# Kernel optimization log

Measured on AMD Instinct MI355X. Metric: run time of the kernel, lower is better.

## Reference

```python
import jax, jax.numpy as jnp
import numpy as np

D_MODEL = 768
D_FF = 2048
N_EXP = 8
TOP_K = 2


def setup_inputs() -> dict:
    key = jax.random.key(0)
    ks = jax.random.split(key, 8)
    s = 0.02
    inputs = jax.random.normal(ks[0], (4, 2048, D_MODEL), dtype=jnp.float32)
    gate_w = jax.random.normal(ks[1], (D_MODEL, N_EXP), dtype=jnp.float32) * s
    w1 = jax.random.normal(ks[2], (N_EXP, D_MODEL, D_FF), dtype=jnp.float32) * s
    w3 = jax.random.normal(ks[3], (N_EXP, D_MODEL, D_FF), dtype=jnp.float32) * s
    w2 = jax.random.normal(ks[4], (N_EXP, D_FF, D_MODEL), dtype=jnp.float32) * s
    sw1 = jax.random.normal(ks[5], (D_MODEL, D_FF), dtype=jnp.float32) * s
    sw3 = jax.random.normal(ks[6], (D_MODEL, D_FF), dtype=jnp.float32) * s
    sw2 = jax.random.normal(ks[7], (D_FF, D_MODEL), dtype=jnp.float32) * s
    return {"inputs": inputs, "gate_w": gate_w, "w1": w1, "w3": w3, "w2": w2,
            "sw1": sw1, "sw3": sw3, "sw2": sw2}


def _swiglu(x, wa, wb, wc):
    # silu(x @ wa) * (x @ wb) @ wc
    return (jax.nn.silu(x @ wa) * (x @ wb)) @ wc


def reference(inputs, gate_w, w1, w3, w2, sw1, sw3, sw2):
    B, T, D = inputs.shape
    x = inputs.reshape(-1, D)                      # [N, D], N = B*T
    logits = x @ gate_w                            # [N, E]
    topk_scores, topk_idx = jax.lax.top_k(logits, TOP_K)  # [N, K]
    probs = jax.nn.softmax(topk_scores.astype(jnp.float32), axis=-1).astype(inputs.dtype)
    # per-token per-expert combine weight: [N, E]
    one_hot = jax.nn.one_hot(topk_idx, N_EXP, dtype=probs.dtype)  # [N, K, E]
    comb = jnp.einsum('nk,nke->ne', probs, one_hot)               # [N, E]
    out = jnp.zeros_like(x)
    for e in range(N_EXP):  # fixed small expert loop
        out = out + comb[:, e:e + 1] * _swiglu(x, w1[e], w3[e], w2[e])
    out = out + _swiglu(x, sw1, sw3, sw2)
    return out.reshape(B, T, D)
```

## Files before the change

### kernel.cpp

```cpp
#include <hip/hip_runtime.h>
#include <hip/hip_bf16.h>

#define N_TOK 8192
#define DM 768
#define DFF 2048
#define NE 8
#define SHARED_BASE 17408
#define TOTAL_ROWS 25600

typedef __attribute__((ext_vector_type(8))) __bf16 bf16x8;
typedef __attribute__((ext_vector_type(4))) float f32x4;

__device__ __forceinline__ unsigned short f2bf(float f) {
  union { float f; unsigned u; } a; a.f = f;
  unsigned r = a.u + 0x7FFFu + ((a.u >> 16) & 1u);
  return (unsigned short)(r >> 16);
}

__device__ __forceinline__ void gload16(const void* g, void* l) {
  __builtin_amdgcn_global_load_lds((const __attribute__((address_space(1))) void*)g,
                                   (__attribute__((address_space(3))) void*)l, 16, 0, 0);
}


__global__ void cvt_x_kernel(const float4* __restrict__ src, ushort4* __restrict__ dst, int n4) {
  int stride = gridDim.x * blockDim.x;
  for (int i = blockIdx.x * blockDim.x + threadIdx.x; i < n4; i += stride) {
    float4 v = src[i];
    ushort4 o;
    o.x = f2bf(v.x); o.y = f2bf(v.y); o.z = f2bf(v.z); o.w = f2bf(v.w);
    dst[i] = o;
  }
}

__global__ void transpose_cvt_kernel(const float* __restrict__ src, unsigned short* __restrict__ dst,
                                     int R, int C) {
  __shared__ float tile[64][65];
  const float* s = src + (size_t)blockIdx.z * R * C;
  unsigned short* d = dst + (size_t)blockIdx.z * R * C;
  int c0 = blockIdx.x * 64, r0 = blockIdx.y * 64;
  int tx = threadIdx.x & 63, ty = threadIdx.x >> 6;
#pragma unroll
  for (int i = 0; i < 16; i++) {
    int row = i * 4 + ty;
    tile[row][tx] = s[(size_t)(r0 + row) * C + c0 + tx];
  }
  __syncthreads();
#pragma unroll
  for (int i = 0; i < 16; i++) {
    int row = i * 4 + ty;
    d[(size_t)(c0 + row) * R + r0 + tx] = f2bf(tile[tx][row]);
  }
}

__global__ __launch_bounds__(256) void gate_kernel(
    const float* __restrict__ x, const float* __restrict__ gw,
    float* __restrict__ probs, int* __restrict__ idxo) {
  __shared__ float gws[8][768];
  const int tid = threadIdx.x;
  for (int i = tid; i < DM * 2; i += 256) {
    float4 v = ((const float4*)gw)[i];
    int dd = i >> 1;
    int e0 = (i & 1) * 4;
    gws[e0 + 0][dd] = v.x; gws[e0 + 1][dd] = v.y;
    gws[e0 + 2][dd] = v.z; gws[e0 + 3][dd] = v.w;
  }
  __syncthreads();
  const int lane = tid & 63, wv = tid >> 6;
  const int tok0 = blockIdx.x * 16 + wv * 4;
  for (int i = 0; i < 4; i++) {
    const int n = tok0 + i;
    const float* xr = x + (size_t)n * DM;
    float xv[12];
#pragma unroll
    for (int it = 0; it < 12; it++) xv[it] = xr[it * 64 + lane];
    double acc[8];
#pragma unroll
    for (int e = 0; e < 8; e++) {
      double a = 0.0;
#pragma unroll
      for (int it = 0; it < 12; it++) a += (double)xv[it] * (double)gws[e][it * 64 + lane];
      acc[e] = a;
    }
#pragma unroll
    for (int off = 32; off > 0; off >>= 1)
#pragma unroll
      for (int e = 0; e < 8; e++) acc[e] += __shfl_xor(acc[e], off);
    if (lane == 0) {
      int e0 = 0; double v0 = acc[0];
#pragma unroll
      for (int e = 1; e < 8; e++) if (acc[e] > v0) { v0 = acc[e]; e0 = e; }
      int e1 = -1; double v1 = -1e300;
#pragma unroll
      for (int e = 0; e < 8; e++) if (e != e0 && acc[e] > v1) { v1 = acc[e]; e1 = e; }
      double p0 = 1.0 / (1.0 + exp(v1 - v0));
      probs[n * 2 + 0] = (float)p0;
      probs[n * 2 + 1] = (float)(1.0 - p0);
      idxo[n * 2 + 0] = e0;
      idxo[n * 2 + 1] = e1;
    }
  }
}

__global__ __launch_bounds__(256) void route_kernel(
    const int* __restrict__ idxo,
    int* __restrict__ cnt, int* __restrict__ offs,
    int* __restrict__ list, int* __restrict__ slt) {
  __shared__ int lcnt[256][8];
  __shared__ int lstart[256][8];
  __shared__ int base[8];
  const int t = threadIdx.x;
#pragma unroll
  for (int e = 0; e < 8; e++) lcnt[t][e] = 0;
  __syncthreads();
  const int i0 = t * 64;
  for (int j = 0; j < 64; j++) {
    int e = idxo[i0 + j];
    lcnt[t][e]++;
  }
  __syncthreads();
  if (t < 8) {
    int run = 0;
    for (int tt = 0; tt < 256; tt++) { lstart[tt][t] = run; run += lcnt[tt][t]; }
    base[t] = run;
  }
  __syncthreads();
  if (t == 0) {
    int cum = 0;
    for (int e = 0; e < 8; e++) {
      int tot = base[e];
      cnt[e] = tot; offs[e] = cum;
      base[e] = cum;
      cum += (tot + 127) & ~127;
    }
    offs[8] = cum;
  }
  __syncthreads();
#pragma unroll
  for (int e = 0; e < 8; e++) lcnt[t][e] = base[e] + lstart[t][e];
  for (int j = 0; j < 64; j++) {
    int i = i0 + j;
    int e = idxo[i];
    int pos = lcnt[t][e]++;
    list[pos] = i >> 1;
    slt[i] = pos;
  }
}

__global__ __launch_bounds__(256, 2) void gemm1_kernel(
    const char* __restrict__ xb,
    const char* __restrict__ w1T,
    const char* __restrict__ w3T,
    const char* __restrict__ sw1T,
    const char* __restrict__ sw3T,
    const int* __restrict__ list, const int* __restrict__ cnt, const int* __restrict__ offs,
    unsigned short* __restrict__ Hb)
{
  __shared__ unsigned short Al[128 * 64];
  __shared__ unsigned short B1l[64 * 64];
  __shared__ unsigned short B3l[64 * 64];

  const int by = blockIdx.y;
  const int f0 = blockIdx.x * 64;
  const int tid = threadIdx.x;
  const int lane = tid & 63;
  const int wv = tid >> 6;
  const int wm = wv >> 1, wn = wv & 1;
  const int wflat = tid & ~63;

  const char *w1p, *w3p;
  int base_slot, tbase, cnt_e, offs_e = 0;
  const bool is_shared = (by >= 512);
  if (!is_shared) {
    int e = by >> 6, t = by & 63;
    cnt_e = cnt[e];
    if (t * 128 >= cnt_e) return;
    offs_e = offs[e];
    base_slot = offs_e + t * 128;
    tbase = t * 128;
    w1p = w1T + (size_t)e * DFF * DM * 2;
    w3p = w3T + (size_t)e * DFF * DM * 2;
  } else {
    int t = by - 512;
    base_slot = SHARED_BASE + t * 128;
    tbase = t * 128;
    cnt_e = 1 << 30;
    w1p = sw1T; w3p = sw3T;
  }

  const int brow = tid >> 3;
  const int bcol = tid & 7;

  size_t abase[4];
#pragma unroll
  for (int it = 0; it < 4; it++) {
    int row = it * 32 + brow;
    int tok;
    if (is_shared) tok = tbase + row;
    else {
      int ie = tbase + row;
      if (ie >= cnt_e) ie = cnt_e - 1;
      tok = list[offs_e + ie];
    }
    abase[it] = (size_t)tok * (DM * 2) + (size_t)((bcol ^ (row & 7)) << 4);
  }
  size_t bbase[2];
#pragma unroll
  for (int it = 0; it < 2; it++) {
    int row = it * 32 + brow;
    bbase[it] = (size_t)(f0 + row) * (DM * 2) + (size_t)((bcol ^ (row & 7)) << 4);
  }

  f32x4 acc1[4][2], acc3[4][2];
  const f32x4 z4 = {0.f, 0.f, 0.f, 0.f};
#pragma unroll
  for (int mi = 0; mi < 4; mi++)
#pragma unroll
    for (int ni = 0; ni < 2; ni++) { acc1[mi][ni] = z4; acc3[mi][ni] = z4; }

  const int ml = lane & 15, kg = lane >> 4;

  for (int ks = 0; ks < 12; ks++) {
#pragma unroll
    for (int it = 0; it < 4; it++)
      gload16(xb + abase[it] + ks * 128, (char*)Al + (size_t)((it * 256 + wflat) * 16));
#pragma unroll
    for (int it = 0; it < 2; it++) {
      gload16(w1p + bbase[it] + ks * 128, (char*)B1l + (size_t)((it * 256 + wflat) * 16));
      gload16(w3p + bbase[it] + ks * 128, (char*)B3l + (size_t)((it * 256 + wflat) * 16));
    }
    __syncthreads();
#pragma unroll
    for (int kk = 0; kk < 2; kk++) {
      const int kblk = kk * 4 + kg;
      bf16x8 af[4], b1f[2], b3f[2];
#pragma unroll
      for (int mi = 0; mi < 4; mi++) {
        int m = wm * 64 + mi * 16 + ml;
        af[mi] = *(const bf16x8*)((const char*)Al + m * 128 + ((kblk ^ (ml & 7)) << 4));
      }
#pragma unroll
      for (int ni = 0; ni < 2; ni++) {
        int nn = wn * 32 + ni * 16 + ml;
        int boff = nn * 128 + ((kblk ^ (ml & 7)) << 4);
        b1f[ni] = *(const bf16x8*)((const char*)B1l + boff);
        b3f[ni] = *(const bf16x8*)((const char*)B3l + boff);
      }
#pragma unroll
      for (int mi = 0; mi < 4; mi++)
#pragma unroll
        for (int ni = 0; ni < 2; ni++) {
          acc1[mi][ni] = __builtin_amdgcn_mfma_f32_16x16x32_bf16(af[mi], b1f[ni], acc1[mi][ni], 0, 0, 0);
          acc3[mi][ni] = __builtin_amdgcn_mfma_f32_16x16x32_bf16(af[mi], b3f[ni], acc3[mi][ni], 0, 0, 0);
        }
    }
    __syncthreads();
  }

#pragma unroll
  for (int mi = 0; mi < 4; mi++) {
#pragma unroll
    for (int ni = 0; ni < 2; ni++) {
#pragma unroll
      for (int r = 0; r < 4; r++) {
        int row = wm * 64 + mi * 16 + (lane >> 4) * 4 + r;
        int col = f0 + wn * 32 + ni * 16 + ml;
        float h1 = acc1[mi][ni][r], h3 = acc3[mi][ni][r];
        float s = h1 / (1.0f + expf(-h1));
        Hb[(size_t)(base_slot + row) * DFF + col] = f2bf(s * h3);
      }
    }
  }
}

__global__ __launch_bounds__(256, 2) void gemm2_kernel(
    const char* __restrict__ Hb,
    const char* __restrict__ w2T,
    const char* __restrict__ sw2T,
    const int* __restrict__ cnt, const int* __restrict__ offs,
    float* __restrict__ Ob,
    float* __restrict__ out)
{
  __shared__ unsigned short Al[128 * 64];
  __shared__ unsigned short Bl[128 * 64];

  const int by = blockIdx.y;
  const int d0 = blockIdx.x * 128;
  const int tid = threadIdx.x;
  const int lane = tid & 63;
  const int wv = tid >> 6;
  const int wm = wv >> 1, wn = wv & 1;
  const int wflat = tid & ~63;

  const char* w2p;
  int base_slot, tbase, cnt_e;
  const bool is_shared = (by >= 512);
  if (!is_shared) {
    int e = by >> 6, t = by & 63;
    cnt_e = cnt[e];
    if (t * 128 >= cnt_e) return;
    base_slot = offs[e] + t * 128;
    tbase = t * 128;
    w2p = w2T + (size_t)e * DM * DFF * 2;
  } else {
    int t = by - 512;
    base_slot = SHARED_BASE + t * 128;
    tbase = t * 128;
    cnt_e = 1 << 30;
    w2p = sw2T;
  }

  const int brow = tid >> 3, bcol = tid & 7;
  size_t abase[4], bbase[4];
#pragma unroll
  for (int it = 0; it < 4; it++) {
    int row = it * 32 + brow;
    abase[it] = (size_t)(base_slot + row) * (DFF * 2) + (size_t)((bcol ^ (row & 7)) << 4);
    bbase[it] = (size_t)(d0 + row) * (DFF * 2) + (size_t)((bcol ^ (row & 7)) << 4);
  }

  f32x4 acc[4][4];
  const f32x4 z4 = {0.f, 0.f, 0.f, 0.f};
#pragma unroll
  for (int mi = 0; mi < 4; mi++)
#pragma unroll
    for (int ni = 0; ni < 4; ni++) acc[mi][ni] = z4;

  const int ml = lane & 15, kg = lane >> 4;

  for (int ks = 0; ks < 32; ks++) {
#pragma unroll
    for (int it = 0; it < 4; it++) {
      gload16(Hb + abase[it] + ks * 128, (char*)Al + (size_t)((it * 256 + wflat) * 16));
      gload16(w2p + bbase[it] + ks * 128, (char*)Bl + (size_t)((it * 256 + wflat) * 16));
    }
    __syncthreads();
#pragma unroll
    for (int kk = 0; kk < 2; kk++) {
      const int kblk = kk * 4 + kg;
      bf16x8 af[4], bfr[4];
#pragma unroll
      for (int mi = 0; mi < 4; mi++) {
        int m = wm * 64 + mi * 16 + ml;
        af[mi] = *(const bf16x8*)((const char*)Al + m * 128 + ((kblk ^ (ml & 7)) << 4));
      }
#pragma unroll
      for (int ni = 0; ni < 4; ni++) {
        int nn = wn * 64 + ni * 16 + ml;
        bfr[ni] = *(const bf16x8*)((const char*)Bl + nn * 128 + ((kblk ^ (ml & 7)) << 4));
      }
#pragma unroll
      for (int mi = 0; mi < 4; mi++)
#pragma unroll
        for (int ni = 0; ni < 4; ni++)
          acc[mi][ni] = __builtin_amdgcn_mfma_f32_16x16x32_bf16(af[mi], bfr[ni], acc[mi][ni], 0, 0, 0);
    }
    __syncthreads();
  }

#pragma unroll
  for (int mi = 0; mi < 4; mi++) {
#pragma unroll
    for (int r = 0; r < 4; r++) {
      int row = wm * 64 + mi * 16 + (lane >> 4) * 4 + r;
      float* orow = is_shared ? (out + (size_t)(tbase + row) * DM + d0)
                              : (Ob + (size_t)(base_slot + row) * DM + d0);
#pragma unroll
      for (int ni = 0; ni < 4; ni++)
        orow[wn * 64 + ni * 16 + ml] = acc[mi][ni][r];
    }
  }
}

__global__ __launch_bounds__(192) void combine_kernel(
    const float4* __restrict__ Ob4, const int* __restrict__ slt,
    const float* __restrict__ probs, float4* __restrict__ out4) {
  const int n = blockIdx.x;
  const int t = threadIdx.x;
  const int s0 = slt[2 * n], s1 = slt[2 * n + 1];
  const float p0 = probs[2 * n], p1 = probs[2 * n + 1];
  float4 a = out4[(size_t)n * 192 + t];
  float4 b = Ob4[(size_t)s0 * 192 + t];
  float4 c = Ob4[(size_t)s1 * 192 + t];
  a.x += p0 * b.x + p1 * c.x;
  a.y += p0 * b.y + p1 * c.y;
  a.z += p0 * b.z + p1 * c.z;
  a.w += p0 * b.w + p1 * c.w;
  out4[(size_t)n * 192 + t] = a;
}


extern "C" void kernel_launch(void* const* d_in, const int* in_sizes, int n_in,
                              void* d_out, int out_size, void* d_ws, size_t ws_size,
                              hipStream_t stream) {
  const float* x   = (const float*)d_in[0];
  const float* gw  = (const float*)d_in[1];
  const float* w1  = (const float*)d_in[2];
  const float* w3  = (const float*)d_in[3];
  const float* w2  = (const float*)d_in[4];
  const float* sw1 = (const float*)d_in[5];
  const float* sw3 = (const float*)d_in[6];
  const float* sw2 = (const float*)d_in[7];
  float* out = (float*)d_out;
  char* ws = (char*)d_ws;

  char* xb   = ws;
  char* w2T  = xb + 12582912;
  char* sw2T = w2T + 25165824;
  char* U    = sw2T + 3145728;
  char* w1T  = U;
  char* w3T  = w1T + 25165824;
  char* sw1T = w3T + 25165824;
  char* sw3T = sw1T + 3145728;
  char* Ob   = U;
  char* Hb   = U + 56623104;
  char* probs= Hb + 104857600;
  char* idxo = probs + 65536;
  char* lst  = idxo + 65536;
  char* slt  = lst + 69632;
  char* cntb = slt + 69632;
  char* offb = cntb + 64;

  cvt_x_kernel<<<2048, 256, 0, stream>>>((const float4*)x, (ushort4*)xb, N_TOK * DM / 4);
  transpose_cvt_kernel<<<dim3(32, 12, 8), 256, 0, stream>>>(w1, (unsigned short*)w1T, DM, DFF);
  transpose_cvt_kernel<<<dim3(32, 12, 8), 256, 0, stream>>>(w3, (unsigned short*)w3T, DM, DFF);
  transpose_cvt_kernel<<<dim3(12, 32, 8), 256, 0, stream>>>(w2, (unsigned short*)w2T, DFF, DM);
  transpose_cvt_kernel<<<dim3(32, 12, 1), 256, 0, stream>>>(sw1, (unsigned short*)sw1T, DM, DFF);
  transpose_cvt_kernel<<<dim3(32, 12, 1), 256, 0, stream>>>(sw3, (unsigned short*)sw3T, DM, DFF);
  transpose_cvt_kernel<<<dim3(12, 32, 1), 256, 0, stream>>>(sw2, (unsigned short*)sw2T, DFF, DM);

  gate_kernel<<<512, 256, 0, stream>>>(x, gw, (float*)probs, (int*)idxo);
  route_kernel<<<1, 256, 0, stream>>>((const int*)idxo,
                                      (int*)cntb, (int*)offb, (int*)lst, (int*)slt);

  gemm1_kernel<<<dim3(32, 576), 256, 0, stream>>>(xb, w1T, w3T, sw1T, sw3T,
      (const int*)lst, (const int*)cntb, (const int*)offb, (unsigned short*)Hb);

  gemm2_kernel<<<dim3(6, 576), 256, 0, stream>>>(Hb, w2T, sw2T,
      (const int*)cntb, (const int*)offb, (float*)Ob, out);

  combine_kernel<<<N_TOK, 192, 0, stream>>>((const float4*)Ob, (const int*)slt,
                                            (const float*)probs, (float4*)out);
}
```

Measured before the change: 433.6 us.

## Add 4-stage LDS pipelining to both MoE GEMMs and enlarge gemm1 tiles

Both expert GEMMs now use a 4-buffer LDS ring with direct global-to-LDS loads issued three K-steps ahead. Completion is tracked with explicit vmcnt waits and one barrier per step, which replaces the load/sync/compute/sync loop. gemm1 moves to 512-thread blocks covering 256 tokens by 128 FF columns, with w1 and w3 interleaved into a single B tile, so each x tile is reused across more MFMAs. It also skips Hb writes beyond the padded count. The cost is 128KB of LDS per gemm1 block, which limits occupancy, and a large register footprint for the accumulators.

```diff
diff --git a/kernel.cpp b/kernel.cpp
--- a/kernel.cpp
+++ b/kernel.cpp
@@ -147,7 +147,7 @@
   }
 }
 
-__global__ __launch_bounds__(256, 2) void gemm1_kernel(
+__global__ __launch_bounds__(512, 2) void gemm1_kernel(
     const char* __restrict__ xb,
     const char* __restrict__ w1T,
     const char* __restrict__ w3T,
@@ -156,45 +156,46 @@
     const int* __restrict__ list, const int* __restrict__ cnt, const int* __restrict__ offs,
     unsigned short* __restrict__ Hb)
 {
-  __shared__ unsigned short Al[128 * 64];
-  __shared__ unsigned short B1l[64 * 64];
-  __shared__ unsigned short B3l[64 * 64];
+  __shared__ __attribute__((aligned(128))) unsigned char lds[4][32768];
 
   const int by = blockIdx.y;
-  const int f0 = blockIdx.x * 64;
+  const int f0 = blockIdx.x * 128;
   const int tid = threadIdx.x;
   const int lane = tid & 63;
   const int wv = tid >> 6;
-  const int wm = wv >> 1, wn = wv & 1;
+  const int wm = wv >> 1;
+  const int wn = wv & 1;
   const int wflat = tid & ~63;
+  const int ml = lane & 15, kg = lane >> 4;
 
   const char *w1p, *w3p;
-  int base_slot, tbase, cnt_e, offs_e = 0;
-  const bool is_shared = (by >= 512);
+  int base_slot, tbase, cnt_e, cnt_pad = 1 << 30, offs_e = 0;
+  const bool is_shared = (by >= 256);
   if (!is_shared) {
-    int e = by >> 6, t = by & 63;
+    int e = by >> 5, t = by & 31;
     cnt_e = cnt[e];
-    if (t * 128 >= cnt_e) return;
+    if (t * 256 >= cnt_e) return;
+    cnt_pad = (cnt_e + 127) & ~127;
     offs_e = offs[e];
-    base_slot = offs_e + t * 128;
-    tbase = t * 128;
+    base_slot = offs_e + t * 256;
+    tbase = t * 256;
     w1p = w1T + (size_t)e * DFF * DM * 2;
     w3p = w3T + (size_t)e * DFF * DM * 2;
   } else {
-    int t = by - 512;
-    base_slot = SHARED_BASE + t * 128;
-    tbase = t * 128;
+    int t = by - 256;
+    base_slot = SHARED_BASE + t * 256;
+    tbase = t * 256;
     cnt_e = 1 << 30;
     w1p = sw1T; w3p = sw3T;
   }
 
-  const int brow = tid >> 3;
-  const int bcol = tid & 7;
-
-  size_t abase[4];
-#pragma unroll
-  for (int it = 0; it < 4; it++) {
-    int row = it * 32 + brow;
+  size_t asrc[2];
+  const char* bsrc[2];
+#pragma unroll
+  for (int it = 0; it < 2; it++) {
+    int g = it * 512 + tid;
+    int row = g >> 2;
+    int schk = (g & 3) ^ ((row >> 1) & 3);
     int tok;
     if (is_shared) tok = tbase + row;
     else {
@@ -202,72 +203,81 @@
       if (ie >= cnt_e) ie = cnt_e - 1;
       tok = list[offs_e + ie];
     }
-    abase[it] = (size_t)tok * (DM * 2) + (size_t)((bcol ^ (row & 7)) << 4);
-  }
-  size_t bbase[2];
-#pragma unroll
-  for (int it = 0; it < 2; it++) {
-    int row = it * 32 + brow;
-    bbase[it] = (size_t)(f0 + row) * (DM * 2) + (size_t)((bcol ^ (row & 7)) << 4);
-  }
-
-  f32x4 acc1[4][2], acc3[4][2];
+    asrc[it] = (size_t)tok * (DM * 2) + (size_t)(schk << 4);
+    int mat = (row >> 6) & 1;
+    int fcol = f0 + ((row >> 7) << 6) + (row & 63);
+    bsrc[it] = (mat ? w3p : w1p) + (size_t)fcol * (DM * 2) + (size_t)(schk << 4);
+  }
+
+  int aoff[4], boff[8];
+#pragma unroll
+  for (int mi = 0; mi < 4; mi++) {
+    int m = wm * 64 + mi * 16 + ml;
+    aoff[mi] = (m * 4 + (kg ^ ((m >> 1) & 3))) << 4;
+  }
+#pragma unroll
+  for (int nj = 0; nj < 8; nj++) {
+    int r = wn * 128 + nj * 16 + ml;
+    boff[nj] = 16384 + ((r * 4 + (kg ^ ((r >> 1) & 3))) << 4);
+  }
+
+  f32x4 acc[4][8];
   const f32x4 z4 = {0.f, 0.f, 0.f, 0.f};
 #pragma unroll
   for (int mi = 0; mi < 4; mi++)
 #pragma unroll
-    for (int ni = 0; ni < 2; ni++) { acc1[mi][ni] = z4; acc3[mi][ni] = z4; }
-
-  const int ml = lane & 15, kg = lane >> 4;
-
-  for (int ks = 0; ks < 12; ks++) {
-#pragma unroll
-    for (int it = 0; it < 4; it++)
-      gload16(xb + abase[it] + ks * 128, (char*)Al + (size_t)((it * 256 + wflat) * 16));
-#pragma unroll
-    for (int it = 0; it < 2; it++) {
-      gload16(w1p + bbase[it] + ks * 128, (char*)B1l + (size_t)((it * 256 + wflat) * 16));
-      gload16(w3p + bbase[it] + ks * 128, (char*)B3l + (size_t)((it * 256 + wflat) * 16));
-    }
-    __syncthreads();
-#pragma unroll
-    for (int kk = 0; kk < 2; kk++) {
-      const int kblk = kk * 4 + kg;
-      bf16x8 af[4], b1f[2], b3f[2];
-#pragma unroll
-      for (int mi = 0; mi < 4; mi++) {
-        int m = wm * 64 + mi * 16 + ml;
-        af[mi] = *(const bf16x8*)((const char*)Al + m * 128 + ((kblk ^ (ml & 7)) << 4));
-      }
-#pragma unroll
-      for (int ni = 0; ni < 2; ni++) {
-        int nn = wn * 32 + ni * 16 + ml;
-        int boff = nn * 128 + ((kblk ^ (ml & 7)) << 4);
-        b1f[ni] = *(const bf16x8*)((const char*)B1l + boff);
-        b3f[ni] = *(const bf16x8*)((const char*)B3l + boff);
-      }
-#pragma unroll
-      for (int mi = 0; mi < 4; mi++)
-#pragma unroll
-        for (int ni = 0; ni < 2; ni++) {
-          acc1[mi][ni] = __builtin_amdgcn_mfma_f32_16x16x32_bf16(af[mi], b1f[ni], acc1[mi][ni], 0, 0, 0);
-          acc3[mi][ni] = __builtin_amdgcn_mfma_f32_16x16x32_bf16(af[mi], b3f[ni], acc3[mi][ni], 0, 0, 0);
-        }
-    }
-    __syncthreads();
-  }
+    for (int nj = 0; nj < 8; nj++) acc[mi][nj] = z4;
+
+#define G1_STAGE(kt, b) {                                                    \
+    char* Lb_ = (char*)lds[b];                                               \
+    gload16(xb + asrc[0] + (kt) * 64, Lb_ + (size_t)((0 * 512 + wflat) * 16)); \
+    gload16(xb + asrc[1] + (kt) * 64, Lb_ + (size_t)((1 * 512 + wflat) * 16)); \
+    gload16(bsrc[0] + (kt) * 64, Lb_ + 16384 + (size_t)((0 * 512 + wflat) * 16)); \
+    gload16(bsrc[1] + (kt) * 64, Lb_ + 16384 + (size_t)((1 * 512 + wflat) * 16)); \
+  }
+
+  G1_STAGE(0, 0);
+  G1_STAGE(1, 1);
+  G1_STAGE(2, 2);
+
+  const int KT = 24;
+  for (int t = 0; t < KT; t++) {
+    if (t < KT - 2)      { asm volatile("s_waitcnt vmcnt(8)" ::: "memory"); }
+    else if (t == KT - 2){ asm volatile("s_waitcnt vmcnt(4)" ::: "memory"); }
+    else                 { asm volatile("s_waitcnt vmcnt(0)" ::: "memory"); }
+    __builtin_amdgcn_sched_barrier(0);
+    __builtin_amdgcn_s_barrier();
+    __builtin_amdgcn_sched_barrier(0);
+    if (t + 3 < KT) G1_STAGE(t + 3, (t + 3) & 3);
+
+    const char* Ab = (const char*)lds[t & 3];
+    bf16x8 af[4], bfr[8];
+#pragma unroll
+    for (int mi = 0; mi < 4; mi++) af[mi] = *(const bf16x8*)(Ab + aoff[mi]);
+#pragma unroll
+    for (int nj = 0; nj < 8; nj++) bfr[nj] = *(const bf16x8*)(Ab + boff[nj]);
+    __builtin_amdgcn_s_setprio(1);
+#pragma unroll
+    for (int mi = 0; mi < 4; mi++)
+#pragma unroll
+      for (int nj = 0; nj < 8; nj++)
+        acc[mi][nj] = __builtin_amdgcn_mfma_f32_16x16x32_bf16(af[mi], bfr[nj], acc[mi][nj], 0, 0, 0);
+    __builtin_amdgcn_s_setprio(0);
+  }
+#undef G1_STAGE
 
 #pragma unroll
   for (int mi = 0; mi < 4; mi++) {
 #pragma unroll
-    for (int ni = 0; ni < 2; ni++) {
-#pragma unroll
-      for (int r = 0; r < 4; r++) {
-        int row = wm * 64 + mi * 16 + (lane >> 4) * 4 + r;
-        int col = f0 + wn * 32 + ni * 16 + ml;
-        float h1 = acc1[mi][ni][r], h3 = acc3[mi][ni][r];
+    for (int r = 0; r < 4; r++) {
+      int row = wm * 64 + mi * 16 + (lane >> 4) * 4 + r;
+      if (!is_shared && tbase + row >= cnt_pad) continue;
+      size_t hrow = (size_t)(base_slot + row) * DFF;
+#pragma unroll
+      for (int nj = 0; nj < 4; nj++) {
+        float h1 = acc[mi][nj][r], h3 = acc[mi][nj + 4][r];
         float s = h1 / (1.0f + expf(-h1));
-        Hb[(size_t)(base_slot + row) * DFF + col] = f2bf(s * h3);
+        Hb[hrow + f0 + wn * 64 + nj * 16 + ml] = f2bf(s * h3);
       }
     }
   }
@@ -281,16 +291,17 @@
     float* __restrict__ Ob,
     float* __restrict__ out)
 {
-  __shared__ unsigned short Al[128 * 64];
-  __shared__ unsigned short Bl[128 * 64];
+  __shared__ __attribute__((aligned(128))) unsigned char lds[4][16384];
 
   const int by = blockIdx.y;
   const int d0 = blockIdx.x * 128;
   const int tid = threadIdx.x;
   const int lane = tid & 63;
   const int wv = tid >> 6;
-  const int wm = wv >> 1, wn = wv & 1;
+  const int wm = wv >> 1;
+  const int wn = wv & 1;
   const int wflat = tid & ~63;
+  const int ml = lane & 15, kg = lane >> 4;
 
   const char* w2p;
   int base_slot, tbase, cnt_e;
@@ -310,13 +321,27 @@
     w2p = sw2T;
   }
 
-  const int brow = tid >> 3, bcol = tid & 7;
-  size_t abase[4], bbase[4];
-#pragma unroll
-  for (int it = 0; it < 4; it++) {
-    int row = it * 32 + brow;
-    abase[it] = (size_t)(base_slot + row) * (DFF * 2) + (size_t)((bcol ^ (row & 7)) << 4);
-    bbase[it] = (size_t)(d0 + row) * (DFF * 2) + (size_t)((bcol ^ (row & 7)) << 4);
+  size_t asrc[2];
+  const char* bsrc[2];
+#pragma unroll
+  for (int it = 0; it < 2; it++) {
+    int g = it * 256 + tid;
+    int row = g >> 2;
+    int schk = (g & 3) ^ ((row >> 1) & 3);
+    asrc[it] = (size_t)(base_slot + row) * (DFF * 2) + (size_t)(schk << 4);
+    bsrc[it] = w2p + (size_t)(d0 + row) * (DFF * 2) + (size_t)(schk << 4);
+  }
+
+  int aoff[4], boff[4];
+#pragma unroll
+  for (int mi = 0; mi < 4; mi++) {
+    int m = wm * 64 + mi * 16 + ml;
+    aoff[mi] = (m * 4 + (kg ^ ((m >> 1) & 3))) << 4;
+  }
+#pragma unroll
+  for (int nj = 0; nj < 4; nj++) {
+    int r = wn * 64 + nj * 16 + ml;
+    boff[nj] = 8192 + ((r * 4 + (kg ^ ((r >> 1) & 3))) << 4);
   }
 
   f32x4 acc[4][4];
@@ -324,39 +349,45 @@
 #pragma unroll
   for (int mi = 0; mi < 4; mi++)
 #pragma unroll
-    for (int ni = 0; ni < 4; ni++) acc[mi][ni] = z4;
-
-  const int ml = lane & 15, kg = lane >> 4;
-
-  for (int ks = 0; ks < 32; ks++) {
-#pragma unroll
-    for (int it = 0; it < 4; it++) {
-      gload16(Hb + abase[it] + ks * 128, (char*)Al + (size_t)((it * 256 + wflat) * 16));
-      gload16(w2p + bbase[it] + ks * 128, (char*)Bl + (size_t)((it * 256 + wflat) * 16));
-    }
-    __syncthreads();
-#pragma unroll
-    for (int kk = 0; kk < 2; kk++) {
-      const int kblk = kk * 4 + kg;
-      bf16x8 af[4], bfr[4];
-#pragma unroll
-      for (int mi = 0; mi < 4; mi++) {
-        int m = wm * 64 + mi * 16 + ml;
-        af[mi] = *(const bf16x8*)((const char*)Al + m * 128 + ((kblk ^ (ml & 7)) << 4));
-      }
-#pragma unroll
-      for (int ni = 0; ni < 4; ni++) {
-        int nn = wn * 64 + ni * 16 + ml;
-        bfr[ni] = *(const bf16x8*)((const char*)Bl + nn * 128 + ((kblk ^ (ml & 7)) << 4));
-      }
-#pragma unroll
-      for (int mi = 0; mi < 4; mi++)
-#pragma unroll
-        for (int ni = 0; ni < 4; ni++)
-          acc[mi][ni] = __builtin_amdgcn_mfma_f32_16x16x32_bf16(af[mi], bfr[ni], acc[mi][ni], 0, 0, 0);
-    }
-    __syncthreads();
-  }
+    for (int nj = 0; nj < 4; nj++) acc[mi][nj] = z4;
+
+#define G2_STAGE(kt, b) {                                                    \
+    char* Lb_ = (char*)lds[b];                                               \
+    gload16(Hb + asrc[0] + (kt) * 64, Lb_ + (size_t)((0 * 256 + wflat) * 16)); \
+    gload16(Hb + asrc[1] + (kt) * 64, Lb_ + (size_t)((1 * 256 + wflat) * 16)); \
+    gload16(bsrc[0] + (kt) * 64, Lb_ + 8192 + (size_t)((0 * 256 + wflat) * 16)); \
+    gload16(bsrc[1] + (kt) * 64, Lb_ + 8192 + (size_t)((1 * 256 + wflat) * 16)); \
+  }
+
+  G2_STAGE(0, 0);
+  G2_STAGE(1, 1);
+  G2_STAGE(2, 2);
+
+  const int KT = 64;
+  for (int t = 0; t < KT; t++) {
+    if (t < KT - 2)      { asm volatile("s_waitcnt vmcnt(8)" ::: "memory"); }
+    else if (t == KT - 2){ asm volatile("s_waitcnt vmcnt(4)" ::: "memory"); }
+    else                 { asm volatile("s_waitcnt vmcnt(0)" ::: "memory"); }
+    __builtin_amdgcn_sched_barrier(0);
+    __builtin_amdgcn_s_barrier();
+    __builtin_amdgcn_sched_barrier(0);
+    if (t + 3 < KT) G2_STAGE(t + 3, (t + 3) & 3);
+
+    const char* Ab = (const char*)lds[t & 3];
+    bf16x8 af[4], bfr[4];
+#pragma unroll
+    for (int mi = 0; mi < 4; mi++) af[mi] = *(const bf16x8*)(Ab + aoff[mi]);
+#pragma unroll
+    for (int nj = 0; nj < 4; nj++) bfr[nj] = *(const bf16x8*)(Ab + boff[nj]);
+    __builtin_amdgcn_s_setprio(1);
+#pragma unroll
+    for (int mi = 0; mi < 4; mi++)
+#pragma unroll
+      for (int nj = 0; nj < 4; nj++)
+        acc[mi][nj] = __builtin_amdgcn_mfma_f32_16x16x32_bf16(af[mi], bfr[nj], acc[mi][nj], 0, 0, 0);
+    __builtin_amdgcn_s_setprio(0);
+  }
+#undef G2_STAGE
 
 #pragma unroll
   for (int mi = 0; mi < 4; mi++) {
@@ -366,8 +397,8 @@
       float* orow = is_shared ? (out + (size_t)(tbase + row) * DM + d0)
                               : (Ob + (size_t)(base_slot + row) * DM + d0);
 #pragma unroll
-      for (int ni = 0; ni < 4; ni++)
-        orow[wn * 64 + ni * 16 + ml] = acc[mi][ni][r];
+      for (int nj = 0; nj < 4; nj++)
+        orow[wn * 64 + nj * 16 + ml] = acc[mi][nj][r];
     }
   }
 }
@@ -433,7 +464,7 @@
   route_kernel<<<1, 256, 0, stream>>>((const int*)idxo,
                                       (int*)cntb, (int*)offb, (int*)lst, (int*)slt);
 
-  gemm1_kernel<<<dim3(32, 576), 256, 0, stream>>>(xb, w1T, w3T, sw1T, sw3T,
+  gemm1_kernel<<<dim3(16, 288), 512, 0, stream>>>(xb, w1T, w3T, sw1T, sw3T,
       (const int*)lst, (const int*)cntb, (const int*)offb, (unsigned short*)Hb);
 
   gemm2_kernel<<<dim3(6, 576), 256, 0, stream>>>(Hb, w2T, sw2T,
```

Result: slower. 459.2 us (+5.9%).

## Merge weight transposes into one launch and widen gemm2 tile to 128x256

Applied to the files above, without the earlier changes.

The six weight transpose/convert launches become a single kernel that picks the source tensor from blockIdx.z and early-exits blocks outside each tensor's bounds. gemm2 moves to 512-thread blocks with a 128x256 output tile (8 waves arranged 2x4), so each A tile of H is loaded once per 256 output columns instead of 128. This halves redundant reloads of H and the block count, but raises LDS use per block and launches many empty transpose blocks.

```diff
diff --git a/kernel.cpp b/kernel.cpp
--- a/kernel.cpp
+++ b/kernel.cpp
@@ -33,12 +33,24 @@
   }
 }
 
-__global__ void transpose_cvt_kernel(const float* __restrict__ src, unsigned short* __restrict__ dst,
-                                     int R, int C) {
+__global__ void transpose_all_kernel(
+    const float* __restrict__ w1, const float* __restrict__ w3, const float* __restrict__ w2,
+    const float* __restrict__ sw1, const float* __restrict__ sw3, const float* __restrict__ sw2,
+    unsigned short* __restrict__ w1T, unsigned short* __restrict__ w3T,
+    unsigned short* __restrict__ w2T,
+    unsigned short* __restrict__ sw1T, unsigned short* __restrict__ sw3T,
+    unsigned short* __restrict__ sw2T) {
   __shared__ float tile[64][65];
-  const float* s = src + (size_t)blockIdx.z * R * C;
-  unsigned short* d = dst + (size_t)blockIdx.z * R * C;
+  const int z = blockIdx.z;
+  const float* s; unsigned short* d; int R, C;
+  if (z < 8)       { s = w1 + (size_t)z * DM * DFF;        d = w1T + (size_t)z * DM * DFF;        R = DM;  C = DFF; }
+  else if (z < 16) { s = w3 + (size_t)(z - 8) * DM * DFF;  d = w3T + (size_t)(z - 8) * DM * DFF;  R = DM;  C = DFF; }
+  else if (z < 24) { s = w2 + (size_t)(z - 16) * DFF * DM; d = w2T + (size_t)(z - 16) * DFF * DM; R = DFF; C = DM;  }
+  else if (z == 24){ s = sw1; d = sw1T; R = DM;  C = DFF; }
+  else if (z == 25){ s = sw3; d = sw3T; R = DM;  C = DFF; }
+  else             { s = sw2; d = sw2T; R = DFF; C = DM;  }
   int c0 = blockIdx.x * 64, r0 = blockIdx.y * 64;
+  if (c0 >= C || r0 >= R) return;
   int tx = threadIdx.x & 63, ty = threadIdx.x >> 6;
 #pragma unroll
   for (int i = 0; i < 16; i++) {
@@ -273,7 +285,7 @@
   }
 }
 
-__global__ __launch_bounds__(256, 2) void gemm2_kernel(
+__global__ __launch_bounds__(512, 4) void gemm2_kernel(
     const char* __restrict__ Hb,
     const char* __restrict__ w2T,
     const char* __restrict__ sw2T,
@@ -282,14 +294,15 @@
     float* __restrict__ out)
 {
   __shared__ unsigned short Al[128 * 64];
-  __shared__ unsigned short Bl[128 * 64];
+  __shared__ unsigned short Bl[256 * 64];
 
   const int by = blockIdx.y;
-  const int d0 = blockIdx.x * 128;
+  const int d0 = blockIdx.x * 256;
   const int tid = threadIdx.x;
   const int lane = tid & 63;
   const int wv = tid >> 6;
-  const int wm = wv >> 1, wn = wv & 1;
+  const int wm = wv >> 2;
+  const int wn = wv & 3;
   const int wflat = tid & ~63;
 
   const char* w2p;
@@ -311,11 +324,15 @@
   }
 
   const int brow = tid >> 3, bcol = tid & 7;
-  size_t abase[4], bbase[4];
+  size_t abase[2], bbase[4];
+#pragma unroll
+  for (int it = 0; it < 2; it++) {
+    int row = it * 64 + brow;
+    abase[it] = (size_t)(base_slot + row) * (DFF * 2) + (size_t)((bcol ^ (row & 7)) << 4);
+  }
 #pragma unroll
   for (int it = 0; it < 4; it++) {
-    int row = it * 32 + brow;
-    abase[it] = (size_t)(base_slot + row) * (DFF * 2) + (size_t)((bcol ^ (row & 7)) << 4);
+    int row = it * 64 + brow;
     bbase[it] = (size_t)(d0 + row) * (DFF * 2) + (size_t)((bcol ^ (row & 7)) << 4);
   }
 
@@ -324,16 +341,17 @@
 #pragma unroll
   for (int mi = 0; mi < 4; mi++)
 #pragma unroll
-    for (int ni = 0; ni < 4; ni++) acc[mi][ni] = z4;
+    for (int nj = 0; nj < 4; nj++) acc[mi][nj] = z4;
 
   const int ml = lane & 15, kg = lane >> 4;
 
   for (int ks = 0; ks < 32; ks++) {
 #pragma unroll
-    for (int it = 0; it < 4; it++) {
-      gload16(Hb + abase[it] + ks * 128, (char*)Al + (size_t)((it * 256 + wflat) * 16));
-      gload16(w2p + bbase[it] + ks * 128, (char*)Bl + (size_t)((it * 256 + wflat) * 16));
-    }
+    for (int it = 0; it < 2; it++)
+      gload16(Hb + abase[it] + ks * 128, (char*)Al + (size_t)((it * 512 + tid) * 16));
+#pragma unroll
+    for (int it = 0; it < 4; it++)
+      gload16(w2p + bbase[it] + ks * 128, (char*)Bl + (size_t)((it * 512 + tid) * 16));
     __syncthreads();
 #pragma unroll
     for (int kk = 0; kk < 2; kk++) {
@@ -345,15 +363,15 @@
         af[mi] = *(const bf16x8*)((const char*)Al + m * 128 + ((kblk ^ (ml & 7)) << 4));
       }
 #pragma unroll
-      for (int ni = 0; ni < 4; ni++) {
-        int nn = wn * 64 + ni * 16 + ml;
-        bfr[ni] = *(const bf16x8*)((const char*)Bl + nn * 128 + ((kblk ^ (ml & 7)) << 4));
+      for (int nj = 0; nj < 4; nj++) {
+        int nn = wn * 64 + nj * 16 + ml;
+        bfr[nj] = *(const bf16x8*)((const char*)Bl + nn * 128 + ((kblk ^ (ml & 7)) << 4));
       }
 #pragma unroll
       for (int mi = 0; mi < 4; mi++)
 #pragma unroll
-        for (int ni = 0; ni < 4; ni++)
-          acc[mi][ni] = __builtin_amdgcn_mfma_f32_16x16x32_bf16(af[mi], bfr[ni], acc[mi][ni], 0, 0, 0);
+        for (int nj = 0; nj < 4; nj++)
+          acc[mi][nj] = __builtin_amdgcn_mfma_f32_16x16x32_bf16(af[mi], bfr[nj], acc[mi][nj], 0, 0, 0);
     }
     __syncthreads();
   }
@@ -366,8 +384,8 @@
       float* orow = is_shared ? (out + (size_t)(tbase + row) * DM + d0)
                               : (Ob + (size_t)(base_slot + row) * DM + d0);
 #pragma unroll
-      for (int ni = 0; ni < 4; ni++)
-        orow[wn * 64 + ni * 16 + ml] = acc[mi][ni][r];
+      for (int nj = 0; nj < 4; nj++)
+        orow[wn * 64 + nj * 16 + ml] = acc[mi][nj][r];
     }
   }
 }
@@ -422,12 +440,10 @@
   char* offb = cntb + 64;
 
   cvt_x_kernel<<<2048, 256, 0, stream>>>((const float4*)x, (ushort4*)xb, N_TOK * DM / 4);
-  transpose_cvt_kernel<<<dim3(32, 12, 8), 256, 0, stream>>>(w1, (unsigned short*)w1T, DM, DFF);
-  transpose_cvt_kernel<<<dim3(32, 12, 8), 256, 0, stream>>>(w3, (unsigned short*)w3T, DM, DFF);
-  transpose_cvt_kernel<<<dim3(12, 32, 8), 256, 0, stream>>>(w2, (unsigned short*)w2T, DFF, DM);
-  transpose_cvt_kernel<<<dim3(32, 12, 1), 256, 0, stream>>>(sw1, (unsigned short*)sw1T, DM, DFF);
-  transpose_cvt_kernel<<<dim3(32, 12, 1), 256, 0, stream>>>(sw3, (unsigned short*)sw3T, DM, DFF);
-  transpose_cvt_kernel<<<dim3(12, 32, 1), 256, 0, stream>>>(sw2, (unsigned short*)sw2T, DFF, DM);
+  transpose_all_kernel<<<dim3(32, 32, 27), 256, 0, stream>>>(
+      w1, w3, w2, sw1, sw3, sw2,
+      (unsigned short*)w1T, (unsigned short*)w3T, (unsigned short*)w2T,
+      (unsigned short*)sw1T, (unsigned short*)sw3T, (unsigned short*)sw2T);
 
   gate_kernel<<<512, 256, 0, stream>>>(x, gw, (float*)probs, (int*)idxo);
   route_kernel<<<1, 256, 0, stream>>>((const int*)idxo,
@@ -436,7 +452,7 @@
   gemm1_kernel<<<dim3(32, 576), 256, 0, stream>>>(xb, w1T, w3T, sw1T, sw3T,
       (const int*)lst, (const int*)cntb, (const int*)offb, (unsigned short*)Hb);
 
-  gemm2_kernel<<<dim3(6, 576), 256, 0, stream>>>(Hb, w2T, sw2T,
+  gemm2_kernel<<<dim3(3, 576), 512, 0, stream>>>(Hb, w2T, sw2T,
       (const int*)cntb, (const int*)offb, (float*)Ob, out);
 
   combine_kernel<<<N_TOK, 192, 0, stream>>>((const float4*)Ob, (const int*)slt,
```

Measured after the change: 390.1 us. 10.0% less time.
